# Performance work log

Measured on AMD Instinct MI355X. Metric: run time of the kernel, lower is better.

## Reference

```python
import jax, jax.numpy as jnp
import numpy as np

ALPHA = 0.5      # GCN2Conv alpha
THETA = 1.0      # GCN2Conv theta (beta_l = log(theta/l + 1))
EPS = 1e-5       # pyg LayerNorm eps
N_LAYERS = 8
N, E, DIN, DHID, DOUT = 50000, 800000, 128, 256, 128


def setup_inputs() -> dict:
    key = jax.random.key(0)
    ks = jax.random.split(key, 10)
    x = jax.random.normal(ks[0], (N, DIN), jnp.float32)
    edge_index = jax.random.randint(ks[1], (2, E), 0, N, dtype=jnp.int32)
    lin1_w = jax.random.normal(ks[2], (DIN, DHID), jnp.float32) / np.sqrt(DIN)
    lin1_b = jnp.zeros((DHID,), jnp.float32)
    conv_w1 = jax.random.normal(ks[3], (N_LAYERS, DHID, DHID), jnp.float32) / np.sqrt(DHID)
    conv_w2 = jax.random.normal(ks[4], (N_LAYERS, DHID, DHID), jnp.float32) / np.sqrt(DHID)
    norm_gamma = jnp.ones((N_LAYERS, DHID), jnp.float32)
    norm_beta = jnp.zeros((N_LAYERS, DHID), jnp.float32)
    lin2_w = jax.random.normal(ks[5], (DHID, DOUT), jnp.float32) / np.sqrt(DHID)
    lin2_b = jnp.zeros((DOUT,), jnp.float32)
    return {"x": x, "edge_index": edge_index, "lin1_w": lin1_w, "lin1_b": lin1_b,
            "conv_w1": conv_w1, "conv_w2": conv_w2, "norm_gamma": norm_gamma,
            "norm_beta": norm_beta, "lin2_w": lin2_w, "lin2_b": lin2_b}


def _gcn_norm(edge_index, n_nodes, dtype):
    # add self loops, then symmetric deg^{-1/2} A_hat deg^{-1/2} normalization
    loop = jnp.arange(n_nodes, dtype=edge_index.dtype)
    row = jnp.concatenate([edge_index[0], loop])
    col = jnp.concatenate([edge_index[1], loop])
    deg = jax.ops.segment_sum(jnp.ones_like(row, dtype=dtype), col, num_segments=n_nodes)
    dis = jnp.where(deg > 0, jax.lax.rsqrt(jnp.maximum(deg, 1e-12)), 0.0)
    return row, col, dis[row] * dis[col]


def _graph_layernorm(h, gamma, beta):
    # pyg LayerNorm mode='graph', batch=None: normalize over all nodes+features
    z = h - jnp.mean(h)
    z = z / (jnp.sqrt(jnp.mean(z * z)) + EPS)
    return gamma * z + beta


def reference(x, edge_index, lin1_w, lin1_b, conv_w1, conv_w2, norm_gamma, norm_beta, lin2_w, lin2_b):
    n_nodes = x.shape[0]
    row, col, enorm = _gcn_norm(edge_index, n_nodes, x.dtype)
    # lin1 + relu (dropout p=0 -> identity); residual=None -> zeros
    x0 = jax.nn.relu(x @ lin1_w + lin1_b)
    h = x0
    for i in range(conv_w1.shape[0]):
        beta_l = float(np.log(THETA / (i + 1) + 1.0))
        # sparse neighborhood aggregation: out[c] += norm * h[r]
        agg = jax.ops.segment_sum(h[row] * enorm[:, None], col, num_segments=n_nodes)
        t = (1.0 - ALPHA) * agg          # propagated part
        r = ALPHA * x0                   # initial-residual part (res = x0 + zeros)
        # shared_weights=False: separate weights for propagated and residual parts
        h = (1.0 - beta_l) * (t + r) + beta_l * (t @ conv_w1[i] + r @ conv_w2[i])
        h = jax.nn.relu(_graph_layernorm(h, norm_gamma[i], norm_beta[i]))
    return jax.nn.relu(h @ lin2_w + lin2_b)
```

## Files before the change

### kernel.cpp

```cpp
#include <hip/hip_runtime.h>
#include <hip/hip_bf16.h>
#include <math.h>

#define DIN 128
#define DH 256
#define DOUT 128
#define NLAYERS 8
#define EPSLN 1e-5f

typedef __hip_bfloat16 bf16;
typedef __attribute__((ext_vector_type(8))) short short8;
typedef __attribute__((ext_vector_type(4))) short short4v;
typedef __attribute__((ext_vector_type(4))) float f32x4;

__device__ __forceinline__ float ldf(const void* p, size_t idx, int isbf) {
    if (isbf) return __bfloat162float(((const bf16*)p)[idx]);
    return ((const float*)p)[idx];
}
__device__ __forceinline__ short f2s(float v) {
    bf16 b = __float2bfloat16(v);
    return *reinterpret_cast<short*>(&b);
}
__device__ __forceinline__ float s2f(short s) {
    unsigned int u = ((unsigned int)(unsigned short)s) << 16;
    float f;
    __builtin_memcpy(&f, &u, 4);
    return f;
}
__device__ __forceinline__ void gl_lds16(const void* g, void* l) {
    __builtin_amdgcn_global_load_lds(
        (const __attribute__((address_space(1))) unsigned int*)g,
        (__attribute__((address_space(3))) unsigned int*)l,
        16, 0, 0);
}

__global__ void k_detect(const unsigned int* __restrict__ xw, int* __restrict__ flag) {
    __shared__ int cnt;
    if (threadIdx.x == 0) cnt = 0;
    __syncthreads();
    unsigned int w = xw[threadIdx.x];
    int e = (w >> 7) & 0xFF;
    if (e >= 112 && e <= 140) atomicAdd(&cnt, 1);
    __syncthreads();
    if (threadIdx.x == 0) *flag = (cnt >= 128) ? 1 : 0;
}

__global__ void k_init_cnt(int* __restrict__ cnt, int N) {
    int i = blockIdx.x * blockDim.x + threadIdx.x;
    if (i < N) cnt[i] = 0;
}
__global__ void k_count(const int* __restrict__ cols, int* __restrict__ cnt, int E) {
    int e = blockIdx.x * blockDim.x + threadIdx.x;
    if (e < E) atomicAdd(&cnt[cols[e]], 1);
}
__global__ void k_dis(const int* __restrict__ cnt, float* __restrict__ dis, int N) {
    int i = blockIdx.x * blockDim.x + threadIdx.x;
    if (i < N) dis[i] = rsqrtf(1.0f + (float)cnt[i]);
}
__global__ void k_scan1(const int* __restrict__ cnt, int* __restrict__ rowptr,
                        int* __restrict__ bsum, int N) {
    __shared__ int s[256];
    int t = threadIdx.x;
    int i = blockIdx.x * 256 + t;
    s[t] = (i < N) ? cnt[i] : 0;
    __syncthreads();
    for (int off = 1; off < 256; off <<= 1) {
        int x = (t >= off) ? s[t - off] : 0;
        __syncthreads();
        s[t] += x;
        __syncthreads();
    }
    if (i < N) rowptr[i + 1] = s[t];
    if (t == 255) bsum[blockIdx.x] = s[255];
}
__global__ void k_scan2(int* __restrict__ bsum, int nb) {
    __shared__ int s[256];
    int t = threadIdx.x;
    s[t] = (t < nb) ? bsum[t] : 0;
    __syncthreads();
    for (int off = 1; off < 256; off <<= 1) {
        int x = (t >= off) ? s[t - off] : 0;
        __syncthreads();
        s[t] += x;
        __syncthreads();
    }
    if (t < nb) bsum[t] = s[t];
}
__global__ void k_scan3(int* __restrict__ rowptr, const int* __restrict__ bsum, int N) {
    int i = blockIdx.x * 256 + threadIdx.x;
    if (i == 0) rowptr[0] = 0;
    if (i < N && blockIdx.x > 0) rowptr[i + 1] += bsum[blockIdx.x - 1];
}
__global__ void k_cursor(const int* __restrict__ rowptr, int* __restrict__ cursor, int N) {
    int i = blockIdx.x * 256 + threadIdx.x;
    if (i < N) cursor[i] = rowptr[i];
}
__global__ void k_fill(const int* __restrict__ rows, const int* __restrict__ cols,
                       int* __restrict__ cursor, int* __restrict__ csr, int E) {
    int e = blockIdx.x * blockDim.x + threadIdx.x;
    if (e < E) {
        int c = cols[e], r = rows[e];
        int pos = atomicAdd(&cursor[c], 1);
        csr[pos] = r;
    }
}

__global__ void k_zero_stats(float* __restrict__ stats) {
    int t = threadIdx.x;
    if (t < 16) stats[t] = 0.0f;
}

__global__ void k_transw2(const void* __restrict__ w1, const void* __restrict__ w2,
                          const int* __restrict__ flag, short* __restrict__ wt) {
    __shared__ float tile[32][33];
    int z = blockIdx.z;
    int lay = z >> 1, m = z & 1;
    const void* src = m ? w2 : w1;
    size_t sbase = (size_t)lay * 65536;
    short* dst = wt + (size_t)lay * 131072 + (size_t)m * 256;
    float bl = logf(1.0f / (float)(lay + 1) + 1.0f);
    float c0 = 0.5f * (1.0f - bl);
    float c1 = 0.5f * bl;
    int isbf = *flag;
    int tx = threadIdx.x, ty = threadIdx.y;
    int n0 = blockIdx.x * 32, k0 = blockIdx.y * 32;
    #pragma unroll
    for (int i = 0; i < 4; i++) {
        int k = k0 + ty + i * 8;
        tile[ty + i * 8][tx] = ldf(src, sbase + (size_t)k * 256 + n0 + tx, isbf);
    }
    __syncthreads();
    #pragma unroll
    for (int i = 0; i < 4; i++) {
        int n = n0 + ty + i * 8;
        int k = k0 + tx;
        float v = c1 * tile[tx][ty + i * 8];
        if (k == n) v += c0;
        dst[(size_t)n * 512 + k] = f2s(v);
    }
}

__global__ void k_transw_lin(const void* __restrict__ src, const int* __restrict__ flag,
                             short* __restrict__ dst, int K, int Nc) {
    __shared__ float tile[32][33];
    int isbf = *flag;
    int tx = threadIdx.x, ty = threadIdx.y;
    int n0 = blockIdx.x * 32, k0 = blockIdx.y * 32;
    #pragma unroll
    for (int i = 0; i < 4; i++) {
        int k = k0 + ty + i * 8;
        tile[ty + i * 8][tx] = ldf(src, (size_t)k * Nc + n0 + tx, isbf);
    }
    __syncthreads();
    #pragma unroll
    for (int i = 0; i < 4; i++) {
        int n = n0 + ty + i * 8;
        dst[(size_t)n * K + k0 + tx] = f2s(tile[tx][ty + i * 8]);
    }
}

__global__ void k_convx(const void* __restrict__ x, const int* __restrict__ flag,
                        short* __restrict__ xb, int total) {
    int i = blockIdx.x * 256 + threadIdx.x;
    if (i < total) xb[i] = f2s(ldf(x, i, *flag));
}

template<int BN, int KK, int FINAL>
__global__ __launch_bounds__(512, 4) void gemm_mfma(
    const short* __restrict__ A, const short* __restrict__ wt,
    const void* __restrict__ bias, const int* __restrict__ flag,
    void* __restrict__ outp, int Nn)
{
    constexpr int NT = BN / 16;
    constexpr int BROUNDS = BN / 128;
    __shared__ __align__(16) short Atile[128 * 32];
    __shared__ __align__(16) short Btile[BN * 32];
    int t = threadIdx.x;
    int w = t >> 6, lane = t & 63;
    int lr = lane & 15, quad = lane >> 4;
    int row0 = blockIdx.x * 128;
    int sf = t >> 6;
    int srow = lane & 15;
    int skq = lane >> 4;
    f32x4 acc[NT];
    #pragma unroll
    for (int nt = 0; nt < NT; nt++)
        #pragma unroll
        for (int j = 0; j < 4; j++) acc[nt][j] = 0.f;

    for (int kb = 0; kb < KK; kb += 32) {
        int gr = row0 + sf * 16 + srow;
        if (gr >= Nn) gr = Nn - 1;
        gl_lds16(A + (size_t)gr * KK + kb + skq * 8, Atile + (size_t)t * 8);
        #pragma unroll
        for (int r = 0; r < BROUNDS; r++) {
            int n = (sf + r * 8) * 16 + srow;
            gl_lds16(wt + (size_t)n * KK + kb + skq * 8,
                     Btile + (size_t)(t + r * 512) * 8);
        }
        __syncthreads();
        short8 a = *(const short8*)(Atile + w * 512 + lane * 8);
        #pragma unroll
        for (int nt = 0; nt < NT; nt++) {
            short8 bv = *(const short8*)(Btile + nt * 512 + lane * 8);
            acc[nt] = __builtin_amdgcn_mfma_f32_16x16x32_bf16(a, bv, acc[nt], 0, 0, 0);
        }
        __syncthreads();
    }
    const int isbf = *flag;
    #pragma unroll
    for (int nt = 0; nt < NT; nt++) {
        int gc = nt * 16 + lr;
        float bb = ldf(bias, gc, isbf);
        #pragma unroll
        for (int i = 0; i < 4; i++) {
            int gr = row0 + w * 16 + quad * 4 + i;
            if (gr < Nn) {
                float v = acc[nt][i] + bb;
                v = v > 0.f ? v : 0.f;
                size_t off = (size_t)gr * BN + gc;
                if (FINAL) {
                    if (isbf) ((bf16*)outp)[off] = __float2bfloat16(v);
                    else      ((float*)outp)[off] = v;
                } else {
                    ((bf16*)outp)[off] = __float2bfloat16(v);
                }
            }
        }
    }
}

__global__ __launch_bounds__(256) void k_gather2(
    const int* __restrict__ rowptr, const int* __restrict__ csr,
    const float* __restrict__ dis, const bf16* __restrict__ hsrc,
    bf16* __restrict__ agg,
    const void* __restrict__ g, const void* __restrict__ b, size_t loff,
    const float* __restrict__ stats2, float invTotal, int useLN,
    const int* __restrict__ flag, int N)
{
    int gid = blockIdx.x * 256 + threadIdx.x;
    int node = gid >> 6;
    if (node >= N) return;
    int lane = gid & 63;
    int col = lane * 4;
    float cA[4], cB[4];
    if (useLN) {
        int isbf = *flag;
        float mu = stats2[0] * invTotal;
        float var = stats2[1] * invTotal - mu * mu;
        var = var > 0.f ? var : 0.f;
        float inv = 1.0f / (sqrtf(var) + EPSLN);
        #pragma unroll
        for (int j = 0; j < 4; j++) {
            float gg = ldf(g, loff + col + j, isbf);
            float bb = ldf(b, loff + col + j, isbf);
            cA[j] = gg * inv;
            cB[j] = fmaf(-gg * inv, mu, bb);
        }
    } else {
        #pragma unroll
        for (int j = 0; j < 4; j++) { cA[j] = 1.0f; cB[j] = 0.0f; }
    }
    const short* hs = (const short*)hsrc;
    float dc = dis[node];
    float acc[4], acc2[4];
    {
        short4v hv = *(const short4v*)(hs + (size_t)node * DH + col);
        #pragma unroll
        for (int j = 0; j < 4; j++) {
            float v = fmaf(cA[j], s2f(hv[j]), cB[j]);
            v = v > 0.f ? v : 0.f;
            acc[j] = dc * v;
            acc2[j] = 0.f;
        }
    }
    int i = rowptr[node], e1 = rowptr[node + 1];
    for (; i + 4 <= e1; i += 4) {
        int r0 = csr[i], r1 = csr[i + 1], r2 = csr[i + 2], r3 = csr[i + 3];
        float w0 = dis[r0], w1 = dis[r1], w2 = dis[r2], w3 = dis[r3];
        short4v v0 = *(const short4v*)(hs + (size_t)r0 * DH + col);
        short4v v1 = *(const short4v*)(hs + (size_t)r1 * DH + col);
        short4v v2 = *(const short4v*)(hs + (size_t)r2 * DH + col);
        short4v v3 = *(const short4v*)(hs + (size_t)r3 * DH + col);
        #pragma unroll
        for (int j = 0; j < 4; j++) {
            float a0 = fmaf(cA[j], s2f(v0[j]), cB[j]); a0 = a0 > 0.f ? a0 : 0.f;
            float a1 = fmaf(cA[j], s2f(v1[j]), cB[j]); a1 = a1 > 0.f ? a1 : 0.f;
            float a2 = fmaf(cA[j], s2f(v2[j]), cB[j]); a2 = a2 > 0.f ? a2 : 0.f;
            float a3 = fmaf(cA[j], s2f(v3[j]), cB[j]); a3 = a3 > 0.f ? a3 : 0.f;
            acc[j]  = fmaf(w0, a0, acc[j]);
            acc2[j] = fmaf(w1, a1, acc2[j]);
            acc[j]  = fmaf(w2, a2, acc[j]);
            acc2[j] = fmaf(w3, a3, acc2[j]);
        }
    }
    for (; i < e1; i++) {
        int r = csr[i];
        float wr = dis[r];
        short4v v0 = *(const short4v*)(hs + (size_t)r * DH + col);
        #pragma unroll
        for (int j = 0; j < 4; j++) {
            float a0 = fmaf(cA[j], s2f(v0[j]), cB[j]); a0 = a0 > 0.f ? a0 : 0.f;
            acc[j] = fmaf(wr, a0, acc[j]);
        }
    }
    short4v o;
    #pragma unroll
    for (int j = 0; j < 4; j++) o[j] = f2s(dc * (acc[j] + acc2[j]));
    *(short4v*)((short*)agg + (size_t)node * DH + col) = o;
}

__global__ __launch_bounds__(512, 4) void gemm_layer3(
    const bf16* __restrict__ agg, const bf16* __restrict__ x0,
    const short* __restrict__ wt, bf16* __restrict__ h,
    float* __restrict__ stats2, int Nn)
{
    __shared__ __align__(16) short Atile[128 * 32];
    __shared__ __align__(16) short Btile[256 * 32];
    __shared__ float sred[16];
    int t = threadIdx.x;
    int w = t >> 6, lane = t & 63;
    int lr = lane & 15, quad = lane >> 4;
    int row0 = blockIdx.x * 128;
    int sf = t >> 6;
    int srow = lane & 15;
    int skq = lane >> 4;
    f32x4 acc[16];
    #pragma unroll
    for (int nt = 0; nt < 16; nt++)
        #pragma unroll
        for (int j = 0; j < 4; j++) acc[nt][j] = 0.f;

    for (int kb = 0; kb < 512; kb += 32) {
        const short* Asrc = (const short*)((kb < DH) ? agg : x0);
        int ka = (kb & (DH - 1)) + skq * 8;
        int gr = row0 + sf * 16 + srow;
        if (gr >= Nn) gr = Nn - 1;
        gl_lds16(Asrc + (size_t)gr * DH + ka, Atile + (size_t)t * 8);
        #pragma unroll
        for (int r = 0; r < 2; r++) {
            int n = (sf + r * 8) * 16 + srow;
            gl_lds16(wt + (size_t)n * 512 + kb + skq * 8,
                     Btile + (size_t)(t + r * 512) * 8);
        }
        __syncthreads();
        short8 a = *(const short8*)(Atile + w * 512 + lane * 8);
        #pragma unroll
        for (int nt = 0; nt < 16; nt++) {
            short8 bv = *(const short8*)(Btile + nt * 512 + lane * 8);
            acc[nt] = __builtin_amdgcn_mfma_f32_16x16x32_bf16(a, bv, acc[nt], 0, 0, 0);
        }
        __syncthreads();
    }
    float lsum = 0.f, lsq = 0.f;
    #pragma unroll
    for (int nt = 0; nt < 16; nt++) {
        int gc = nt * 16 + lr;
        #pragma unroll
        for (int i = 0; i < 4; i++) {
            int gr = row0 + w * 16 + quad * 4 + i;
            if (gr < Nn) {
                float v = acc[nt][i];
                h[(size_t)gr * DH + gc] = __float2bfloat16(v);
                lsum += v;
                lsq += v * v;
            }
        }
    }
    #pragma unroll
    for (int off = 32; off > 0; off >>= 1) {
        lsum += __shfl_down(lsum, off);
        lsq  += __shfl_down(lsq, off);
    }
    if (lane == 0) { sred[w] = lsum; sred[8 + w] = lsq; }
    __syncthreads();
    if (t == 0) {
        float s0 = 0.f, s1 = 0.f;
        #pragma unroll
        for (int i = 0; i < 8; i++) { s0 += sred[i]; s1 += sred[8 + i]; }
        atomicAdd(&stats2[0], s0);
        atomicAdd(&stats2[1], s1);
    }
}

__global__ void k_applyT(
    bf16* __restrict__ h, const float* __restrict__ stats2, float invTotal,
    const void* __restrict__ g, const void* __restrict__ b, size_t loff,
    const int* __restrict__ flag, int total)
{
    int idx = blockIdx.x * 256 + threadIdx.x;
    if (idx >= total) return;
    const int isbf = *flag;
    float mu = stats2[0] * invTotal;
    float var = stats2[1] * invTotal - mu * mu;
    var = var > 0.f ? var : 0.f;
    float inv = 1.0f / (sqrtf(var) + EPSLN);
    int j = idx & (DH - 1);
    float gg = ldf(g, loff + j, isbf);
    float bb = ldf(b, loff + j, isbf);
    float v = fmaf(gg * inv, __bfloat162float(h[idx]), fmaf(-gg * inv, mu, bb));
    v = v > 0.f ? v : 0.f;
    h[idx] = __float2bfloat16(v);
}

extern "C" void kernel_launch(void* const* d_in, const int* in_sizes, int n_in,
                              void* d_out, int out_size, void* d_ws, size_t ws_size,
                              hipStream_t stream) {
    const void* x      = d_in[0];
    const int*  ei     = (const int*)d_in[1];
    const void* lin1_w = d_in[2];
    const void* lin1_b = d_in[3];
    const void* conv_w1= d_in[4];
    const void* conv_w2= d_in[5];
    const void* gam    = d_in[6];
    const void* bet    = d_in[7];
    const void* lin2_w = d_in[8];
    const void* lin2_b = d_in[9];

    const int N = in_sizes[0] / DIN;
    const int E = in_sizes[1] / 2;
    const int* rows = ei;
    const int* cols = ei + E;
    const size_t NDH = (size_t)N * DH;
    const size_t Nr = ((size_t)N + 255) / 256 * 256;

    char* p = (char*)d_ws;
    auto alloc = [&](size_t bytes) { char* q = p; p += (bytes + 255) & ~(size_t)255; return q; };
    float* dis    = (float*)alloc(Nr * 4);
    float* stats  = (float*)alloc(1024);
    int*   flag   = (int*)(stats + 16);
    int*   cnt    = (int*)alloc(Nr * 4);
    int*   rowptr = (int*)alloc((Nr + 256) * 4);
    int*   cursor = (int*)alloc(Nr * 4);
    int*   bsum   = (int*)alloc(1024);
    int*   csr    = (int*)alloc((size_t)E * 4);
    short* wt     = (short*)alloc((size_t)NLAYERS * 131072 * 2);
    short* w1t    = (short*)alloc((size_t)DH * DIN * 2);
    short* w2t    = (short*)alloc((size_t)DOUT * DH * 2);
    short* xb     = (short*)alloc((size_t)N * DIN * 2);
    bf16*  agg    = (bf16*)alloc(NDH * 2);
    bf16*  x0     = (bf16*)alloc(NDH * 2);
    bf16*  h      = (bf16*)alloc(NDH * 2);

    dim3 blk(256);
    int nbN = (N + 255) / 256;
    dim3 gN(nbN);
    dim3 gE((E + 255) / 256);
    dim3 gB((N + 127) / 128);
    dim3 gG((N + 3) / 4);
    dim3 gElem((unsigned)((NDH + 255) / 256));
    dim3 gTW(8, 8, 16);
    dim3 bTW(32, 8);
    dim3 blk512(512);

    k_detect<<<1, 256, 0, stream>>>((const unsigned int*)x, flag);
    k_init_cnt<<<gN, blk, 0, stream>>>(cnt, N);
    k_count<<<gE, blk, 0, stream>>>(cols, cnt, E);
    k_dis<<<gN, blk, 0, stream>>>(cnt, dis, N);
    k_scan1<<<gN, blk, 0, stream>>>(cnt, rowptr, bsum, N);
    k_scan2<<<1, 256, 0, stream>>>(bsum, nbN);
    k_scan3<<<gN, blk, 0, stream>>>(rowptr, bsum, N);
    k_cursor<<<gN, blk, 0, stream>>>(rowptr, cursor, N);
    k_fill<<<gE, blk, 0, stream>>>(rows, cols, cursor, csr, E);
    k_zero_stats<<<1, 64, 0, stream>>>(stats);
    k_transw2<<<gTW, bTW, 0, stream>>>(conv_w1, conv_w2, flag, wt);
    k_transw_lin<<<dim3(DH / 32, DIN / 32), bTW, 0, stream>>>(lin1_w, flag, w1t, DIN, DH);
    k_transw_lin<<<dim3(DOUT / 32, DH / 32), bTW, 0, stream>>>(lin2_w, flag, w2t, DH, DOUT);
    k_convx<<<dim3((unsigned)(((size_t)N * DIN + 255) / 256)), blk, 0, stream>>>(x, flag, xb, N * DIN);

    gemm_mfma<DH, DIN, 0><<<gB, blk512, 0, stream>>>(xb, w1t, lin1_b, flag, x0, N);

    const float invTotal = 1.0f / ((float)N * (float)DH);
    for (int l = 0; l < NLAYERS; l++) {
        const bf16* hsrc = (l == 0) ? x0 : h;
        size_t loff = (l == 0) ? 0 : (size_t)(l - 1) * DH;
        const float* st = (l == 0) ? stats : stats + 2 * (l - 1);
        k_gather2<<<gG, blk, 0, stream>>>(rowptr, csr, dis, hsrc, agg,
                                          gam, bet, loff, st, invTotal,
                                          l > 0 ? 1 : 0, flag, N);
        gemm_layer3<<<gB, blk512, 0, stream>>>(agg, x0, wt + (size_t)l * 131072,
                                               h, stats + 2 * l, N);
    }
    k_applyT<<<gElem, blk, 0, stream>>>(h, stats + 2 * (NLAYERS - 1), invTotal,
                                        gam, bet, (size_t)(NLAYERS - 1) * DH,
                                        flag, (int)NDH);
    gemm_mfma<DOUT, DH, 1><<<gB, blk512, 0, stream>>>((const short*)h, w2t, lin2_b,
                                                      flag, d_out, N);
}
```

Measured before the change: 1.112 ms.

## Store hidden features in column-sliced layout to localize gather accesses per slice

The GEMM epilogues now write the hidden state (and a copy of x0) in a layout sliced into eight 32-column blocks, each stored contiguously across all nodes. The gather kernel is rewritten so each block handles one slice for 32 nodes, with four lane groups splitting each node's edges and combining results by shuffle. Each slice array is about 3.2 MB, so random neighbour reads are meant to hit in L2 instead of streaming whole 512-byte rows. The cost is narrower 4-byte loads per lane, the CSR being read eight times, an extra x0 copy, and uncoalesced scattered 2-byte stores in the GEMM epilogue.

```diff
diff --git a/kernel.cpp b/kernel.cpp
--- a/kernel.cpp
+++ b/kernel.cpp
@@ -11,6 +11,7 @@
 typedef __hip_bfloat16 bf16;
 typedef __attribute__((ext_vector_type(8))) short short8;
 typedef __attribute__((ext_vector_type(4))) short short4v;
+typedef __attribute__((ext_vector_type(2))) short short2v;
 typedef __attribute__((ext_vector_type(4))) float f32x4;
 
 __device__ __forceinline__ float ldf(const void* p, size_t idx, int isbf) {
@@ -169,7 +170,7 @@
 __global__ __launch_bounds__(512, 4) void gemm_mfma(
     const short* __restrict__ A, const short* __restrict__ wt,
     const void* __restrict__ bias, const int* __restrict__ flag,
-    void* __restrict__ outp, int Nn)
+    void* __restrict__ outp, short* __restrict__ outs, int Nn)
 {
     constexpr int NT = BN / 16;
     constexpr int BROUNDS = BN / 128;
@@ -224,96 +225,87 @@
                     else      ((float*)outp)[off] = v;
                 } else {
                     ((bf16*)outp)[off] = __float2bfloat16(v);
+                    if (outs) {
+                        outs[((size_t)(gc >> 5) * (size_t)Nn + gr) * 32 + (gc & 31)] = f2s(v);
+                    }
                 }
             }
         }
     }
 }
 
-__global__ __launch_bounds__(256) void k_gather2(
+__global__ __launch_bounds__(256) void k_gather3(
     const int* __restrict__ rowptr, const int* __restrict__ csr,
-    const float* __restrict__ dis, const bf16* __restrict__ hsrc,
+    const float* __restrict__ dis, const short* __restrict__ hsrc,
     bf16* __restrict__ agg,
     const void* __restrict__ g, const void* __restrict__ b, size_t loff,
     const float* __restrict__ stats2, float invTotal, int useLN,
     const int* __restrict__ flag, int N)
 {
-    int gid = blockIdx.x * 256 + threadIdx.x;
-    int node = gid >> 6;
-    if (node >= N) return;
-    int lane = gid & 63;
-    int col = lane * 4;
-    float cA[4], cB[4];
+    int s = blockIdx.x & 7;
+    int chunk = blockIdx.x >> 3;
+    int t = threadIdx.x;
+    int w = t >> 6, lane = t & 63;
+    int grp = lane >> 4;
+    int cl = (lane & 15) * 2;
+    int col = s * 32 + cl;
+    float cA0, cA1, cB0, cB1;
     if (useLN) {
         int isbf = *flag;
         float mu = stats2[0] * invTotal;
         float var = stats2[1] * invTotal - mu * mu;
         var = var > 0.f ? var : 0.f;
         float inv = 1.0f / (sqrtf(var) + EPSLN);
-        #pragma unroll
-        for (int j = 0; j < 4; j++) {
-            float gg = ldf(g, loff + col + j, isbf);
-            float bb = ldf(b, loff + col + j, isbf);
-            cA[j] = gg * inv;
-            cB[j] = fmaf(-gg * inv, mu, bb);
-        }
+        float g0 = ldf(g, loff + col, isbf), g1 = ldf(g, loff + col + 1, isbf);
+        float b0 = ldf(b, loff + col, isbf), b1 = ldf(b, loff + col + 1, isbf);
+        cA0 = g0 * inv; cB0 = fmaf(-g0 * inv, mu, b0);
+        cA1 = g1 * inv; cB1 = fmaf(-g1 * inv, mu, b1);
     } else {
-        #pragma unroll
-        for (int j = 0; j < 4; j++) { cA[j] = 1.0f; cB[j] = 0.0f; }
-    }
-    const short* hs = (const short*)hsrc;
-    float dc = dis[node];
-    float acc[4], acc2[4];
-    {
-        short4v hv = *(const short4v*)(hs + (size_t)node * DH + col);
-        #pragma unroll
-        for (int j = 0; j < 4; j++) {
-            float v = fmaf(cA[j], s2f(hv[j]), cB[j]);
-            v = v > 0.f ? v : 0.f;
-            acc[j] = dc * v;
-            acc2[j] = 0.f;
-        }
-    }
-    int i = rowptr[node], e1 = rowptr[node + 1];
-    for (; i + 4 <= e1; i += 4) {
-        int r0 = csr[i], r1 = csr[i + 1], r2 = csr[i + 2], r3 = csr[i + 3];
-        float w0 = dis[r0], w1 = dis[r1], w2 = dis[r2], w3 = dis[r3];
-        short4v v0 = *(const short4v*)(hs + (size_t)r0 * DH + col);
-        short4v v1 = *(const short4v*)(hs + (size_t)r1 * DH + col);
-        short4v v2 = *(const short4v*)(hs + (size_t)r2 * DH + col);
-        short4v v3 = *(const short4v*)(hs + (size_t)r3 * DH + col);
-        #pragma unroll
-        for (int j = 0; j < 4; j++) {
-            float a0 = fmaf(cA[j], s2f(v0[j]), cB[j]); a0 = a0 > 0.f ? a0 : 0.f;
-            float a1 = fmaf(cA[j], s2f(v1[j]), cB[j]); a1 = a1 > 0.f ? a1 : 0.f;
-            float a2 = fmaf(cA[j], s2f(v2[j]), cB[j]); a2 = a2 > 0.f ? a2 : 0.f;
-            float a3 = fmaf(cA[j], s2f(v3[j]), cB[j]); a3 = a3 > 0.f ? a3 : 0.f;
-            acc[j]  = fmaf(w0, a0, acc[j]);
-            acc2[j] = fmaf(w1, a1, acc2[j]);
-            acc[j]  = fmaf(w2, a2, acc[j]);
-            acc2[j] = fmaf(w3, a3, acc2[j]);
-        }
-    }
-    for (; i < e1; i++) {
-        int r = csr[i];
-        float wr = dis[r];
-        short4v v0 = *(const short4v*)(hs + (size_t)r * DH + col);
-        #pragma unroll
-        for (int j = 0; j < 4; j++) {
-            float a0 = fmaf(cA[j], s2f(v0[j]), cB[j]); a0 = a0 > 0.f ? a0 : 0.f;
-            acc[j] = fmaf(wr, a0, acc[j]);
-        }
-    }
-    short4v o;
-    #pragma unroll
-    for (int j = 0; j < 4; j++) o[j] = f2s(dc * (acc[j] + acc2[j]));
-    *(short4v*)((short*)agg + (size_t)node * DH + col) = o;
+        cA0 = cA1 = 1.0f; cB0 = cB1 = 0.0f;
+    }
+    const short* hs = hsrc + (size_t)s * (size_t)N * 32;
+    int node0 = chunk * 32 + w * 8;
+    for (int ni = 0; ni < 8; ni++) {
+        int node = node0 + ni;
+        if (node >= N) break;
+        float dc = dis[node];
+        float a0 = 0.f, a1 = 0.f;
+        if (grp == 0) {
+            short2v hv = *(const short2v*)(hs + (size_t)node * 32 + cl);
+            float v0 = fmaf(cA0, s2f(hv[0]), cB0); v0 = v0 > 0.f ? v0 : 0.f;
+            float v1 = fmaf(cA1, s2f(hv[1]), cB1); v1 = v1 > 0.f ? v1 : 0.f;
+            a0 = dc * v0; a1 = dc * v1;
+        }
+        int ib = rowptr[node], ie = rowptr[node + 1];
+        int i = ib + grp;
+        int rn = (i < ie) ? __builtin_nontemporal_load(csr + i) : 0;
+        while (i < ie) {
+            int r = rn;
+            int i2 = i + 4;
+            if (i2 < ie) rn = __builtin_nontemporal_load(csr + i2);
+            float wr = dis[r];
+            short2v hv = *(const short2v*)(hs + (size_t)r * 32 + cl);
+            float v0 = fmaf(cA0, s2f(hv[0]), cB0); v0 = v0 > 0.f ? v0 : 0.f;
+            float v1 = fmaf(cA1, s2f(hv[1]), cB1); v1 = v1 > 0.f ? v1 : 0.f;
+            a0 = fmaf(wr, v0, a0);
+            a1 = fmaf(wr, v1, a1);
+            i = i2;
+        }
+        a0 += __shfl_xor(a0, 16); a0 += __shfl_xor(a0, 32);
+        a1 += __shfl_xor(a1, 16); a1 += __shfl_xor(a1, 32);
+        if (grp == 0) {
+            short2v o;
+            o[0] = f2s(dc * a0);
+            o[1] = f2s(dc * a1);
+            *(short2v*)((short*)agg + (size_t)node * DH + col) = o;
+        }
+    }
 }
 
 __global__ __launch_bounds__(512, 4) void gemm_layer3(
     const bf16* __restrict__ agg, const bf16* __restrict__ x0,
     const short* __restrict__ wt, bf16* __restrict__ h,
-    float* __restrict__ stats2, int Nn)
+    float* __restrict__ stats2, int sliced, int Nn)
 {
     __shared__ __align__(16) short Atile[128 * 32];
     __shared__ __align__(16) short Btile[256 * 32];
@@ -352,6 +344,7 @@
         }
         __syncthreads();
     }
+    short* hS = (short*)h;
     float lsum = 0.f, lsq = 0.f;
     #pragma unroll
     for (int nt = 0; nt < 16; nt++) {
@@ -361,7 +354,11 @@
             int gr = row0 + w * 16 + quad * 4 + i;
             if (gr < Nn) {
                 float v = acc[nt][i];
-                h[(size_t)gr * DH + gc] = __float2bfloat16(v);
+                if (sliced) {
+                    hS[((size_t)(gc >> 5) * (size_t)Nn + gr) * 32 + (gc & 31)] = f2s(v);
+                } else {
+                    h[(size_t)gr * DH + gc] = __float2bfloat16(v);
+                }
                 lsum += v;
                 lsq += v * v;
             }
@@ -440,6 +437,7 @@
     short* xb     = (short*)alloc((size_t)N * DIN * 2);
     bf16*  agg    = (bf16*)alloc(NDH * 2);
     bf16*  x0     = (bf16*)alloc(NDH * 2);
+    short* x0s    = (short*)alloc(NDH * 2);
     bf16*  h      = (bf16*)alloc(NDH * 2);
 
     dim3 blk(256);
@@ -447,7 +445,7 @@
     dim3 gN(nbN);
     dim3 gE((E + 255) / 256);
     dim3 gB((N + 127) / 128);
-    dim3 gG((N + 3) / 4);
+    dim3 gG((unsigned)(8 * ((N + 31) / 32)));
     dim3 gElem((unsigned)((NDH + 255) / 256));
     dim3 gTW(8, 8, 16);
     dim3 bTW(32, 8);
@@ -468,22 +466,23 @@
     k_transw_lin<<<dim3(DOUT / 32, DH / 32), bTW, 0, stream>>>(lin2_w, flag, w2t, DH, DOUT);
     k_convx<<<dim3((unsigned)(((size_t)N * DIN + 255) / 256)), blk, 0, stream>>>(x, flag, xb, N * DIN);
 
-    gemm_mfma<DH, DIN, 0><<<gB, blk512, 0, stream>>>(xb, w1t, lin1_b, flag, x0, N);
+    gemm_mfma<DH, DIN, 0><<<gB, blk512, 0, stream>>>(xb, w1t, lin1_b, flag, x0, x0s, N);
 
     const float invTotal = 1.0f / ((float)N * (float)DH);
     for (int l = 0; l < NLAYERS; l++) {
-        const bf16* hsrc = (l == 0) ? x0 : h;
+        const short* hsrc = (l == 0) ? x0s : (const short*)h;
         size_t loff = (l == 0) ? 0 : (size_t)(l - 1) * DH;
         const float* st = (l == 0) ? stats : stats + 2 * (l - 1);
-        k_gather2<<<gG, blk, 0, stream>>>(rowptr, csr, dis, hsrc, agg,
+        k_gather3<<<gG, blk, 0, stream>>>(rowptr, csr, dis, hsrc, agg,
                                           gam, bet, loff, st, invTotal,
                                           l > 0 ? 1 : 0, flag, N);
         gemm_layer3<<<gB, blk512, 0, stream>>>(agg, x0, wt + (size_t)l * 131072,
-                                               h, stats + 2 * l, N);
+                                               h, stats + 2 * l,
+                                               (l < NLAYERS - 1) ? 1 : 0, N);
     }
     k_applyT<<<gElem, blk, 0, stream>>>(h, stats + 2 * (NLAYERS - 1), invTotal,
                                         gam, bet, (size_t)(NLAYERS - 1) * DH,
                                         flag, (int)NDH);
     gemm_mfma<DOUT, DH, 1><<<gB, blk512, 0, stream>>>((const short*)h, w2t, lin2_b,
-                                                      flag, d_out, N);
-}
+                                                      flag, d_out, nullptr, N);
+}
```

Measured after the change: 2.203 ms. 1.98x slower.
